# Performance work log

Measured on AMD Instinct MI355X. Metric: run time of the kernel, lower is better.

The kernel has to match this reference:

```python
import jax, jax.numpy as jnp
import numpy as np

N_NODES = 20000
N_EDGES = 640000
D_IN = 128
D_OUT = 128


def _weighted_mean_aggr(x, src, dst, ew, n):
    # mean over incoming edges of (edge_weight * x_src) -> [n, d]
    msg = x[src] * ew[:, None]                          # [E, d]
    s = jax.ops.segment_sum(msg, dst, num_segments=n)   # [n, d]
    cnt = jax.ops.segment_sum(jnp.ones_like(ew), dst, num_segments=n)
    return s / jnp.maximum(cnt, 1.0)[:, None]


def setup_inputs() -> dict:
    key = jax.random.key(0)
    ks = jax.random.split(key, 12)
    scale_x = 1.0 / np.sqrt(D_IN)
    scale_h = 1.0 / np.sqrt(D_OUT)
    return {
        "X": jax.random.normal(ks[0], (N_NODES, D_IN), jnp.float32),
        "edge_index": jax.random.randint(ks[1], (2, N_EDGES), 0, N_NODES),
        "edge_weight": jax.random.uniform(ks[2], (N_EDGES,), jnp.float32),
        "H": jax.random.normal(ks[3], (N_NODES, D_OUT), jnp.float32),
        "C": jax.random.normal(ks[4], (N_NODES, D_OUT), jnp.float32),
        # stacked gate weights, gate order: [i, f, c, o]
        "Wx_l": jax.random.normal(ks[5], (4, D_IN, D_OUT), jnp.float32) * scale_x,
        "Wx_r": jax.random.normal(ks[6], (4, D_IN, D_OUT), jnp.float32) * scale_x,
        "bx": jnp.zeros((4, D_OUT), jnp.float32),
        "Wh_l": jax.random.normal(ks[7], (4, D_OUT, D_OUT), jnp.float32) * scale_h,
        "Wh_r": jax.random.normal(ks[8], (4, D_OUT, D_OUT), jnp.float32) * scale_h,
        "bh": jnp.zeros((4, D_OUT), jnp.float32),
        # peephole weights, order [i, f, o]
        "wc": jax.random.normal(ks[9], (3, D_OUT), jnp.float32) * scale_h,
        "bg": jnp.zeros((4, D_OUT), jnp.float32),
    }


def reference(X, edge_index, edge_weight, H, C, Wx_l, Wx_r, bx, Wh_l, Wh_r, bh, wc, bg):
    n = X.shape[0]
    src, dst = edge_index[0], edge_index[1]

    # Shared weighted-mean aggregations (identical graph for all 8 convs)
    aggX = _weighted_mean_aggr(X, src, dst, edge_weight, n)   # [N, D_IN]
    aggH = _weighted_mean_aggr(H, src, dst, edge_weight, n)   # [N, D_OUT]

    # WeightedSAGEConv per gate: lin_l(aggr) + lin_r(x) + bias; stacked over 4 gates
    Gx = jnp.einsum('nd,gdo->gno', aggX, Wx_l) + jnp.einsum('nd,gdo->gno', X, Wx_r) + bx[:, None, :]
    Gh = jnp.einsum('nd,gdo->gno', aggH, Wh_l) + jnp.einsum('nd,gdo->gno', H, Wh_r) + bh[:, None, :]
    G = Gx + Gh                                               # [4, N, D_OUT], order i,f,c,o

    I = jax.nn.sigmoid(G[0] + wc[0] * C + bg[0])
    F = jax.nn.sigmoid(G[1] + wc[1] * C + bg[1])
    T = jnp.tanh(G[2] + bg[2])
    C_new = F * C + I * T
    O = jax.nn.sigmoid(G[3] + wc[2] * C_new + bg[3])
    H_new = O * jnp.tanh(C_new)
    return (H_new, C_new)
```

## Files before the change

### kernel.cpp

```cpp
#include <hip/hip_runtime.h>
#include <math.h>

#define NN 20000
#define NE 640000
#define D  128
#define NSLICE 2500
#define NTILES 625
#define SEG 128
#define NCHUNK 640
#define CHUNK 1000

typedef __attribute__((ext_vector_type(8))) short short8;
typedef __attribute__((ext_vector_type(4))) float floatx4;

static __device__ __forceinline__ unsigned short f2bf(float f) {
    union { float f; unsigned int u; } v; v.f = f;
    unsigned int u = v.u;
    u += 0x7fff + ((u >> 16) & 1);
    return (unsigned short)(u >> 16);
}
static __device__ __forceinline__ unsigned int pack2bf(float a, float b) {
    return (unsigned int)f2bf(a) | ((unsigned int)f2bf(b) << 16);
}
static __device__ __forceinline__ float bf_lo(unsigned int u) {
    union { unsigned int i; float f; } v; v.i = u << 16; return v.f;
}
static __device__ __forceinline__ float bf_hi(unsigned int u) {
    union { unsigned int i; float f; } v; v.i = u & 0xffff0000u; return v.f;
}
static __device__ __forceinline__ float sigm(float x) { return 1.f / (1.f + __expf(-x)); }
static __device__ __forceinline__ float tanhx(float x) { return 1.f - 2.f / (__expf(2.f * x) + 1.f); }

static __device__ __forceinline__ void load_lds16(const void* g, void* l) {
    __builtin_amdgcn_global_load_lds(
        (const __attribute__((address_space(1))) unsigned int*)g,
        (__attribute__((address_space(3))) unsigned int*)l, 16, 0, 0);
}

__global__ void __launch_bounds__(256)
prep_fill_kernel(const int* __restrict__ src, const int* __restrict__ dst,
                 const float* __restrict__ ew, int* __restrict__ cnt,
                 unsigned int* __restrict__ s_p,
                 const float4* __restrict__ X4, const float4* __restrict__ H4,
                 unsigned int* __restrict__ XH32,
                 const float* __restrict__ Wx_l, const float* __restrict__ Wx_r,
                 const float* __restrict__ Wh_l, const float* __restrict__ Wh_r,
                 const float* __restrict__ bx, const float* __restrict__ bh,
                 const float* __restrict__ bg,
                 unsigned short* __restrict__ Wsz, float* __restrict__ bias) {
    int tid = threadIdx.x, b = blockIdx.x;

    int chunk = b >> 3, s = b & 7;
    int lo = s * NSLICE, hi = lo + NSLICE;
    int4 d4, sr4; float4 w4;
    bool fill = (tid < 250);
    if (fill) {
        int e0 = chunk * CHUNK + tid * 4;
        d4  = *(const int4*)(dst + e0);
        sr4 = *(const int4*)(src + e0);
        w4  = *(const float4*)(ew + e0);
    }

    if (b < 2560) {
        int t = b * 256 + tid;
        if (t < NE) {
            float4 x = X4[t];
            float4 h = H4[t];
            int n = t >> 5, q = t & 31;
            unsigned int* row = XH32 + n * 128;
            row[2 * q]          = pack2bf(x.x, x.y);
            row[2 * q + 1]      = pack2bf(x.z, x.w);
            row[64 + 2 * q]     = pack2bf(h.x, h.y);
            row[64 + 2 * q + 1] = pack2bf(h.z, h.w);
        }
    } else if (b < 2816) {
        int t = (b - 2560) * 256 + tid;
        int row = t >> 5;
        int g = row >> 9, k = row & 511;
        int o = (t & 31) * 4;
        const float* Wb; int kk;
        if (k < 128)      { Wb = Wx_l; kk = k; }
        else if (k < 256) { Wb = Wx_r; kk = k - 128; }
        else if (k < 384) { Wb = Wh_l; kk = k - 256; }
        else              { Wb = Wh_r; kk = k - 384; }
        float4 w = *(const float4*)(Wb + g * 16384 + kk * 128 + o);
        int ci = k >> 5, jg = (k >> 3) & 3, off = k & 7;
        unsigned short* wp = Wsz + ci * 16384 + jg * 4096 + (g * 128 + o) * 8 + off;
        wp[0]  = f2bf(w.x);
        wp[8]  = f2bf(w.y);
        wp[16] = f2bf(w.z);
        wp[24] = f2bf(w.w);
        if (k == 0) {
            int j0 = g * 128 + o;
#pragma unroll
            for (int i = 0; i < 4; ++i)
                bias[j0 + i] = bx[j0 + i] + bh[j0 + i] + bg[j0 + i];
        }
    }

    if (fill) {
        int dv[4] = {d4.x, d4.y, d4.z, d4.w};
        int sv[4] = {sr4.x, sr4.y, sr4.z, sr4.w};
        float wv[4] = {w4.x, w4.y, w4.z, w4.w};
#pragma unroll
        for (int k = 0; k < 4; ++k) {
            int d = dv[k];
            if (d >= lo && d < hi) {
                int p = atomicAdd(&cnt[d], 1);
                if (p < SEG)
                    s_p[d * SEG + p] = (unsigned int)sv[k] | ((unsigned int)f2bf(wv[k]) << 16);
            }
        }
    }
}

__global__ void __launch_bounds__(256)
aggregate_kernel(const uint2* __restrict__ XH64,
                 const int* __restrict__ cnt,
                 const unsigned int* __restrict__ s_p,
                 uint2* __restrict__ AGG64) {
    int wv = threadIdx.x >> 6, lane = threadIdx.x & 63;
    int b = blockIdx.x;
    int s = b & 7, j = b >> 3;
    int n = s * NSLICE + j * 4 + wv;
    int deg = cnt[n];
    int m = (deg < SEG) ? deg : SEG;
    const unsigned int* seg = s_p + (size_t)n * SEG;
    float a0 = 0.f, a1 = 0.f, a2 = 0.f, a3 = 0.f;
    int i = 0;
    for (; i + 16 <= m; i += 16) {
        unsigned int e[16];
        uint2 u[16];
#pragma unroll
        for (int k = 0; k < 16; ++k) e[k] = seg[i + k];
#pragma unroll
        for (int k = 0; k < 16; ++k) u[k] = XH64[(size_t)(e[k] & 0xffff) * 64 + lane];
#pragma unroll
        for (int k = 0; k < 16; ++k) {
            float w = __int_as_float(e[k] & 0xffff0000u);
            a0 += bf_lo(u[k].x) * w;
            a1 += bf_hi(u[k].x) * w;
            a2 += bf_lo(u[k].y) * w;
            a3 += bf_hi(u[k].y) * w;
        }
    }
    for (; i + 4 <= m; i += 4) {
        unsigned int e[4];
        uint2 u[4];
#pragma unroll
        for (int k = 0; k < 4; ++k) e[k] = seg[i + k];
#pragma unroll
        for (int k = 0; k < 4; ++k) u[k] = XH64[(size_t)(e[k] & 0xffff) * 64 + lane];
#pragma unroll
        for (int k = 0; k < 4; ++k) {
            float w = __int_as_float(e[k] & 0xffff0000u);
            a0 += bf_lo(u[k].x) * w;
            a1 += bf_hi(u[k].x) * w;
            a2 += bf_lo(u[k].y) * w;
            a3 += bf_hi(u[k].y) * w;
        }
    }
    for (; i < m; ++i) {
        unsigned int e = seg[i];
        float w = __int_as_float(e & 0xffff0000u);
        uint2 u = XH64[(size_t)(e & 0xffff) * 64 + lane];
        a0 += bf_lo(u.x) * w;
        a1 += bf_hi(u.x) * w;
        a2 += bf_lo(u.y) * w;
        a3 += bf_hi(u.y) * w;
    }
    float inv = (deg > 0) ? 1.0f / (float)deg : 1.0f;
    uint2 r;
    r.x = pack2bf(a0 * inv, a1 * inv);
    r.y = pack2bf(a2 * inv, a3 * inv);
    AGG64[(size_t)n * 64 + lane] = r;
}

__global__ void __launch_bounds__(256)
gemm_lstm_kernel(const unsigned short* __restrict__ XH,
                 const unsigned short* __restrict__ AGG,
                 const unsigned short* __restrict__ Wsz,
                 const float* __restrict__ bias,
                 const float* __restrict__ wc,
                 const float* __restrict__ C,
                 float* __restrict__ out) {
    __shared__ __align__(16) short Bs[2][8192];

    int tid = threadIdx.x;
    int wv = tid >> 6, lane = tid & 63;
    int lm = lane & 15, lq = lane >> 4;
    int bid = blockIdx.x;
    int m0 = (bid >> 1) * 32;
    int hb = (bid & 1) * 512;

    floatx4 acc[2][4];
#pragma unroll
    for (int mt = 0; mt < 2; ++mt)
#pragma unroll
        for (int g = 0; g < 4; ++g) acc[mt][g] = (floatx4)(0.f);

#pragma unroll
    for (int g = 0; g < 4; ++g)
        load_lds16(Wsz + wv * 4096 + g * 1024 + hb + lane * 8,
                   &Bs[0][wv * 2048 + g * 512]);

    short8 ca0, ca1;
    {
        const unsigned short* ar = AGG + (size_t)(m0 + lm) * 256 + lq * 8;
        ca0 = *(const short8*)ar;
        ca1 = *(const short8*)(ar + 16 * 256);
    }

    for (int it = 0; it < 16; ++it) {
        __syncthreads();
        if (it < 15) {
            const unsigned short* wb = Wsz + (it + 1) * 16384 + wv * 4096 + hb;
            short* lb = &Bs[(it + 1) & 1][wv * 2048];
#pragma unroll
            for (int g = 0; g < 4; ++g)
                load_lds16(wb + g * 1024 + lane * 8, &lb[g * 512]);
        }
        short8 na0, na1;
        if (it < 15) {
            int kn = (it + 1) * 32;
            const unsigned short* ab = (kn & 128) ? XH : AGG;
            int aoff = (kn & 127) | ((kn & 256) >> 1);
            const unsigned short* arn = ab + (size_t)(m0 + lm) * 256 + aoff + lq * 8;
            na0 = *(const short8*)arn;
            na1 = *(const short8*)(arn + 16 * 256);
        }
        const short* bsc = Bs[it & 1];
#pragma unroll
        for (int g = 0; g < 4; ++g) {
            short8 bfr = *(const short8*)&bsc[(lq << 11) + (g << 9) + ((wv << 4) + lm) * 8];
            acc[0][g] = __builtin_amdgcn_mfma_f32_16x16x32_bf16(ca0, bfr, acc[0][g], 0, 0, 0);
            acc[1][g] = __builtin_amdgcn_mfma_f32_16x16x32_bf16(ca1, bfr, acc[1][g], 0, 0, 0);
        }
        ca0 = na0; ca1 = na1;
    }

    int cg0 = (hb >> 3) + (wv << 4) + lm;
    float bG[4], wP[3];
#pragma unroll
    for (int g = 0; g < 4; ++g) bG[g] = bias[(g << 7) + cg0];
#pragma unroll
    for (int j = 0; j < 3; ++j) wP[j] = wc[j * 128 + cg0];

#pragma unroll
    for (int mt = 0; mt < 2; ++mt)
#pragma unroll
        for (int r = 0; r < 4; ++r) {
            int row = m0 + mt * 16 + lq * 4 + r;
            float c = C[(size_t)row * D + cg0];
            float pi = acc[mt][0][r] + bG[0] + wP[0] * c;
            float pf = acc[mt][1][r] + bG[1] + wP[1] * c;
            float pt = acc[mt][2][r] + bG[2];
            float po = acc[mt][3][r] + bG[3];
            float I = sigm(pi);
            float F = sigm(pf);
            float T = tanhx(pt);
            float cn = F * c + I * T;
            float O = sigm(po + wP[2] * cn);
            out[(size_t)row * D + cg0] = O * tanhx(cn);
            out[(size_t)NN * D + (size_t)row * D + cg0] = cn;
        }
}

extern "C" void kernel_launch(void* const* d_in, const int* in_sizes, int n_in,
                              void* d_out, int out_size, void* d_ws, size_t ws_size,
                              hipStream_t stream) {
    const float* X  = (const float*)d_in[0];
    const int* ei   = (const int*)d_in[1];
    const float* ew = (const float*)d_in[2];
    const float* H  = (const float*)d_in[3];
    const float* C  = (const float*)d_in[4];
    const float* Wx_l = (const float*)d_in[5];
    const float* Wx_r = (const float*)d_in[6];
    const float* bx   = (const float*)d_in[7];
    const float* Wh_l = (const float*)d_in[8];
    const float* Wh_r = (const float*)d_in[9];
    const float* bh   = (const float*)d_in[10];
    const float* wc   = (const float*)d_in[11];
    const float* bg   = (const float*)d_in[12];
    float* out = (float*)d_out;

    const int* src = ei;
    const int* dst = ei + NE;

    char* ws = (char*)d_ws;
    int* cnt = (int*)(ws + 0);
    unsigned int* s_p = (unsigned int*)(ws + 80128);
    unsigned short* XH  = (unsigned short*)(ws + 10320128);
    unsigned short* AGG = (unsigned short*)(ws + 20560128);
    unsigned short* Wsz = (unsigned short*)(ws + 30800128);
    float* bias = (float*)(ws + 31324416);

    hipMemsetAsync(cnt, 0, NN * sizeof(int), stream);
    prep_fill_kernel<<<5120, 256, 0, stream>>>(src, dst, ew, cnt, s_p,
                                               (const float4*)X, (const float4*)H,
                                               (unsigned int*)XH,
                                               Wx_l, Wx_r, Wh_l, Wh_r,
                                               bx, bh, bg, Wsz, bias);
    aggregate_kernel<<<NN / 4, 256, 0, stream>>>((const uint2*)XH, cnt, s_p,
                                                 (uint2*)AGG);
    gemm_lstm_kernel<<<NTILES * 2, 256, 0, stream>>>(XH, AGG, Wsz, bias, wc, C, out);
}
```

Baseline: 207.3 us.

## Split aggregation across feature quarters and edge groups with shuffle reduction

The aggregate kernel now assigns each 64-lane wave one quarter (64 features) of a node's 256-wide row. Its four 16-lane groups handle different edges in parallel and are combined with xor shuffles at the end. The grid grows from 5000 to 20000 blocks to cover the four feature quarters. The goal is more memory-level parallelism and occupancy for the gather, in exchange for 128-byte segments per edge instead of a full 512-byte row, repeated reads of each node's edge list, and shuffle overhead.

```diff
diff --git a/kernel.cpp b/kernel.cpp
--- a/kernel.cpp
+++ b/kernel.cpp
@@ -115,42 +115,32 @@
 }
 
 __global__ void __launch_bounds__(256)
-aggregate_kernel(const uint2* __restrict__ XH64,
+aggregate_kernel(const unsigned short* __restrict__ XH,
                  const int* __restrict__ cnt,
                  const unsigned int* __restrict__ s_p,
-                 uint2* __restrict__ AGG64) {
+                 unsigned short* __restrict__ AGG) {
     int wv = threadIdx.x >> 6, lane = threadIdx.x & 63;
-    int b = blockIdx.x;
-    int s = b & 7, j = b >> 3;
+    int grp = lane >> 4, fl = lane & 15;
+    int bid = blockIdx.x;
+    int q = bid / 5000;
+    int b2 = bid - q * 5000;
+    int s = b2 & 7, j = b2 >> 3;
     int n = s * NSLICE + j * 4 + wv;
     int deg = cnt[n];
     int m = (deg < SEG) ? deg : SEG;
     const unsigned int* seg = s_p + (size_t)n * SEG;
+    const unsigned short* base = XH + q * 64 + fl * 4;
+
     float a0 = 0.f, a1 = 0.f, a2 = 0.f, a3 = 0.f;
     int i = 0;
     for (; i + 16 <= m; i += 16) {
-        unsigned int e[16];
-        uint2 u[16];
-#pragma unroll
-        for (int k = 0; k < 16; ++k) e[k] = seg[i + k];
-#pragma unroll
-        for (int k = 0; k < 16; ++k) u[k] = XH64[(size_t)(e[k] & 0xffff) * 64 + lane];
-#pragma unroll
-        for (int k = 0; k < 16; ++k) {
-            float w = __int_as_float(e[k] & 0xffff0000u);
-            a0 += bf_lo(u[k].x) * w;
-            a1 += bf_hi(u[k].x) * w;
-            a2 += bf_lo(u[k].y) * w;
-            a3 += bf_hi(u[k].y) * w;
-        }
-    }
-    for (; i + 4 <= m; i += 4) {
         unsigned int e[4];
         uint2 u[4];
 #pragma unroll
-        for (int k = 0; k < 4; ++k) e[k] = seg[i + k];
-#pragma unroll
-        for (int k = 0; k < 4; ++k) u[k] = XH64[(size_t)(e[k] & 0xffff) * 64 + lane];
+        for (int k = 0; k < 4; ++k) e[k] = seg[i + k * 4 + grp];
+#pragma unroll
+        for (int k = 0; k < 4; ++k)
+            u[k] = *(const uint2*)(base + (size_t)(e[k] & 0xffff) * 256);
 #pragma unroll
         for (int k = 0; k < 4; ++k) {
             float w = __int_as_float(e[k] & 0xffff0000u);
@@ -160,20 +150,34 @@
             a3 += bf_hi(u[k].y) * w;
         }
     }
-    for (; i < m; ++i) {
-        unsigned int e = seg[i];
-        float w = __int_as_float(e & 0xffff0000u);
-        uint2 u = XH64[(size_t)(e & 0xffff) * 64 + lane];
-        a0 += bf_lo(u.x) * w;
-        a1 += bf_hi(u.x) * w;
-        a2 += bf_lo(u.y) * w;
-        a3 += bf_hi(u.y) * w;
-    }
-    float inv = (deg > 0) ? 1.0f / (float)deg : 1.0f;
-    uint2 r;
-    r.x = pack2bf(a0 * inv, a1 * inv);
-    r.y = pack2bf(a2 * inv, a3 * inv);
-    AGG64[(size_t)n * 64 + lane] = r;
+    for (; i < m; i += 4) {
+        int idx = i + grp;
+        if (idx < m) {
+            unsigned int e = seg[idx];
+            float w = __int_as_float(e & 0xffff0000u);
+            uint2 u = *(const uint2*)(base + (size_t)(e & 0xffff) * 256);
+            a0 += bf_lo(u.x) * w;
+            a1 += bf_hi(u.x) * w;
+            a2 += bf_lo(u.y) * w;
+            a3 += bf_hi(u.y) * w;
+        }
+    }
+
+#pragma unroll
+    for (int mask = 16; mask < 64; mask <<= 1) {
+        a0 += __shfl_xor(a0, mask, 64);
+        a1 += __shfl_xor(a1, mask, 64);
+        a2 += __shfl_xor(a2, mask, 64);
+        a3 += __shfl_xor(a3, mask, 64);
+    }
+
+    if (grp == 0) {
+        float inv = (deg > 0) ? 1.0f / (float)deg : 1.0f;
+        uint2 r;
+        r.x = pack2bf(a0 * inv, a1 * inv);
+        r.y = pack2bf(a2 * inv, a3 * inv);
+        *(uint2*)(AGG + (size_t)n * 256 + q * 64 + fl * 4) = r;
+    }
 }
 
 __global__ void __launch_bounds__(256)
@@ -301,7 +305,6 @@
                                                (unsigned int*)XH,
                                                Wx_l, Wx_r, Wh_l, Wh_r,
                                                bx, bh, bg, Wsz, bias);
-    aggregate_kernel<<<NN / 4, 256, 0, stream>>>((const uint2*)XH, cnt, s_p,
-                                                 (uint2*)AGG);
+    aggregate_kernel<<<20000, 256, 0, stream>>>(XH, cnt, s_p, AGG);
     gemm_lstm_kernel<<<NTILES * 2, 256, 0, stream>>>(XH, AGG, Wsz, bias, wc, C, out);
 }
```

New measurement: 213.3 us. +2.9%, slower.
